# Kernel tuning notes

Hardware: AMD Instinct MI355X
Metric: run time of the kernel (lower is better)

## Reference

```python
import jax, jax.numpy as jnp
import numpy as np

N = 50000
E = 800000
IN_DIM, HID_DIM, EMB_DIM = 128, 256, 128


def _sage_conv(x, src, dst, Wp, bp, Wl, bl, Wr):
    # PyG SAGEConv(project=True, aggr='max'):
    #   x_proj = relu(x @ Wp + bp)            # projection before message passing
    #   aggr   = scatter_max(x_proj[src] -> dst)  (empty segments -> 0)
    #   out    = aggr @ Wl + bl + x @ Wr      # lin_l(aggr) + lin_r(root)
    x_proj = jax.nn.relu(x @ Wp + bp)                      # [N, in]
    msg = x_proj[src]                                      # [E, in] gather
    aggr = jax.ops.segment_max(msg, dst, num_segments=N)   # [N, in] scatter-max
    aggr = jnp.where(jnp.isneginf(aggr), 0.0, aggr)        # empty neighborhoods -> 0
    return aggr @ Wl + bl + x @ Wr


def setup_inputs() -> dict:
    key = jax.random.key(0)
    ks = jax.random.split(key, 12)
    s = 0.05
    return {
        "x": jax.random.normal(ks[0], (N, IN_DIM), dtype=jnp.float32),
        "edge_index": jax.random.randint(ks[1], (2, E), 0, N, dtype=jnp.int64),
        # layer 1 params
        "Wp1": jax.random.normal(ks[2], (IN_DIM, IN_DIM), dtype=jnp.float32) * s,
        "bp1": jnp.zeros((IN_DIM,), dtype=jnp.float32),
        "Wl1": jax.random.normal(ks[3], (IN_DIM, HID_DIM), dtype=jnp.float32) * s,
        "bl1": jnp.zeros((HID_DIM,), dtype=jnp.float32),
        "Wr1": jax.random.normal(ks[4], (IN_DIM, HID_DIM), dtype=jnp.float32) * s,
        # layer 2 params
        "Wp2": jax.random.normal(ks[5], (HID_DIM, HID_DIM), dtype=jnp.float32) * s,
        "bp2": jnp.zeros((HID_DIM,), dtype=jnp.float32),
        "Wl2": jax.random.normal(ks[6], (HID_DIM, EMB_DIM), dtype=jnp.float32) * s,
        "bl2": jnp.zeros((EMB_DIM,), dtype=jnp.float32),
        "Wr2": jax.random.normal(ks[7], (HID_DIM, EMB_DIM), dtype=jnp.float32) * s,
    }


def reference(x, edge_index, Wp1, bp1, Wl1, bl1, Wr1, Wp2, bp2, Wl2, bl2, Wr2):
    src, dst = edge_index[0], edge_index[1]
    h = jax.nn.relu(_sage_conv(x, src, dst, Wp1, bp1, Wl1, bl1, Wr1))
    h = jax.nn.relu(_sage_conv(h, src, dst, Wp2, bp2, Wl2, bl2, Wr2))
    return h
```

## Files before the change

kernel.cpp:

```cpp
#include <hip/hip_runtime.h>


typedef __attribute__((ext_vector_type(8))) short short8;
typedef __attribute__((ext_vector_type(4))) float f32x4;

#define ADJ_CAP 64

__device__ __forceinline__ unsigned short f2bf(float f) {
    unsigned int u = __float_as_uint(f);
    u += 0x7fffu + ((u >> 16) & 1u);
    return (unsigned short)(u >> 16);
}

__device__ __forceinline__ unsigned int pkmax(unsigned int a, unsigned int b) {
    unsigned int r;
    asm("v_pk_max_u16 %0, %1, %2" : "=v"(r) : "v"(a), "v"(b));
    return r;
}

__device__ __forceinline__ short8 pack8(const float4 f0, const float4 f1) {
    union { unsigned short u[8]; short8 v; } r;
    r.u[0] = f2bf(f0.x); r.u[1] = f2bf(f0.y); r.u[2] = f2bf(f0.z); r.u[3] = f2bf(f0.w);
    r.u[4] = f2bf(f1.x); r.u[5] = f2bf(f1.y); r.u[6] = f2bf(f1.z); r.u[7] = f2bf(f1.w);
    return r.v;
}

__global__ __launch_bounds__(256) void pack_all_kernel(
    const float* __restrict__ Wp1, const float* __restrict__ Wl1,
    const float* __restrict__ Wr1, const float* __restrict__ Wp2,
    const float* __restrict__ Wl2, const float* __restrict__ Wr2,
    unsigned short* __restrict__ P0, unsigned short* __restrict__ P1,
    unsigned short* __restrict__ P2, unsigned short* __restrict__ P3,
    unsigned short* __restrict__ P4, unsigned short* __restrict__ P5)
{
    const int idx = blockIdx.x * 256 + threadIdx.x;
    const float* W; unsigned short* P; int Nc, local;
    if      (idx <  16384) { W = Wp1; P = P0; Nc = 128; local = idx; }
    else if (idx <  49152) { W = Wl1; P = P1; Nc = 256; local = idx - 16384; }
    else if (idx <  81920) { W = Wr1; P = P2; Nc = 256; local = idx - 49152; }
    else if (idx < 147456) { W = Wp2; P = P3; Nc = 256; local = idx - 81920; }
    else if (idx < 180224) { W = Wl2; P = P4; Nc = 128; local = idx - 147456; }
    else if (idx < 212992) { W = Wr2; P = P5; Nc = 128; local = idx - 180224; }
    else return;
    const int k = local / Nc, c = local % Nc;
    P[((size_t)(k >> 3) * Nc + c) * 8 + (k & 7)] = f2bf(W[local]);
}

__global__ __launch_bounds__(256) void build_adj_kernel(
    const int* __restrict__ src, const int* __restrict__ dst,
    int* __restrict__ deg, int* __restrict__ padj, int E)
{
    const int e = blockIdx.x * 256 + threadIdx.x;
    if (e < E) {
        const int d = dst[e];
        const int pos = atomicAdd(&deg[d], 1);
        if (pos < ADJ_CAP) padj[(size_t)d * ADJ_CAP + pos] = src[e];
    }
}

template<int K, bool DUAL, bool A_F32, bool B_F32, bool OUT_BF16>
__global__ __launch_bounds__(256) void gemm_ks(
    const void* __restrict__ Ap, const void* __restrict__ Bp,
    const unsigned short* __restrict__ Wl,
    const unsigned short* __restrict__ Wr,
    const float* __restrict__ bias,
    void* __restrict__ outp, int M, int N)
{
    constexpr int LDK = K + 8;
    constexpr int CH  = K / 8;
    __shared__ unsigned short As[64 * LDK];

    const int tid  = threadIdx.x;
    const int lane = tid & 63;
    const int wave = tid >> 6;
    const int fr   = lane & 15;
    const int g    = lane >> 4;
    const int bm   = blockIdx.x * 64;
    const int bn   = blockIdx.y * 128;
    const int wc   = bn + wave * 32;

    const f32x4 zero = {0.f, 0.f, 0.f, 0.f};
    f32x4 acc[4][2];
#pragma unroll
    for (int m = 0; m < 4; ++m)
#pragma unroll
        for (int n = 0; n < 2; ++n) acc[m][n] = zero;

#pragma unroll
    for (int ph = 0; ph < (DUAL ? 2 : 1); ++ph) {
        if (ph) __syncthreads();
        const bool f32src = ph ? B_F32 : A_F32;
        const void* __restrict__ S = ph ? Bp : Ap;
#pragma unroll
        for (int c = 0; c < K / 32; ++c) {
            const int t = tid + c * 256;
            const int r = t / CH, q = t % CH;
            const int gm = min(bm + r, M - 1);
            short8 v;
            if (f32src) {
                const float* Sf = (const float*)S;
                const float4 f0 = *reinterpret_cast<const float4*>(Sf + (size_t)gm * K + q * 8);
                const float4 f1 = *reinterpret_cast<const float4*>(Sf + (size_t)gm * K + q * 8 + 4);
                v = pack8(f0, f1);
            } else {
                v = *reinterpret_cast<const short8*>((const unsigned short*)S + (size_t)gm * K + q * 8);
            }
            *reinterpret_cast<short8*>(&As[r * LDK + q * 8]) = v;
        }
        __syncthreads();
        const unsigned short* __restrict__ W = ph ? Wr : Wl;
#pragma unroll
        for (int kt = 0; kt < K / 32; ++kt) {
            short8 af[4];
#pragma unroll
            for (int m = 0; m < 4; ++m)
                af[m] = *reinterpret_cast<const short8*>(
                    &As[(m * 16 + fr) * LDK + kt * 32 + g * 8]);
#pragma unroll
            for (int n = 0; n < 2; ++n) {
                const short8 bf = *reinterpret_cast<const short8*>(
                    W + ((size_t)(kt * 4 + g) * N + wc + n * 16 + fr) * 8);
#pragma unroll
                for (int m = 0; m < 4; ++m)
                    acc[m][n] = __builtin_amdgcn_mfma_f32_16x16x32_bf16(
                        af[m], bf, acc[m][n], 0, 0, 0);
            }
        }
    }

    float bv[2];
#pragma unroll
    for (int n = 0; n < 2; ++n) bv[n] = bias[wc + n * 16 + fr];
#pragma unroll
    for (int m = 0; m < 4; ++m)
#pragma unroll
        for (int j = 0; j < 4; ++j) {
            const int row = bm + m * 16 + g * 4 + j;
            if (row < M) {
#pragma unroll
                for (int n = 0; n < 2; ++n) {
                    const float v = fmaxf(acc[m][n][j] + bv[n], 0.f);
                    const size_t o = (size_t)row * N + wc + n * 16 + fr;
                    if (OUT_BF16) ((unsigned short*)outp)[o] = f2bf(v);
                    else          ((float*)outp)[o]          = v;
                }
            }
        }
}

template<int D>
__global__ __launch_bounds__(256) void gather_max_bf16(
    const unsigned short* __restrict__ p, const int* __restrict__ padj,
    const int* __restrict__ deg, unsigned short* __restrict__ aggr, int n)
{
    const int node = (blockIdx.x * 256 + threadIdx.x) >> 6;
    const int lane = threadIdx.x & 63;
    if (node >= n) return;
    int d = deg[node];
    if (d > ADJ_CAP) d = ADJ_CAP;
    const int* __restrict__ a = padj + (size_t)node * ADJ_CAP;

    if (D == 128) {
        const int q  = lane >> 4;
        const int ll = lane & 15;
        uint4 acc = make_uint4(0u, 0u, 0u, 0u);
        for (int e = 0; e < d; e += 16) {
            const int i0 = min(e + q,      d - 1);
            const int i1 = min(e + 4 + q,  d - 1);
            const int i2 = min(e + 8 + q,  d - 1);
            const int i3 = min(e + 12 + q, d - 1);
            const int r0 = a[i0], r1 = a[i1], r2 = a[i2], r3 = a[i3];
            const uint4 v0 = *reinterpret_cast<const uint4*>(p + (size_t)r0 * 128 + ll * 8);
            const uint4 v1 = *reinterpret_cast<const uint4*>(p + (size_t)r1 * 128 + ll * 8);
            const uint4 v2 = *reinterpret_cast<const uint4*>(p + (size_t)r2 * 128 + ll * 8);
            const uint4 v3 = *reinterpret_cast<const uint4*>(p + (size_t)r3 * 128 + ll * 8);
            acc.x = pkmax(acc.x, pkmax(pkmax(v0.x, v1.x), pkmax(v2.x, v3.x)));
            acc.y = pkmax(acc.y, pkmax(pkmax(v0.y, v1.y), pkmax(v2.y, v3.y)));
            acc.z = pkmax(acc.z, pkmax(pkmax(v0.z, v1.z), pkmax(v2.z, v3.z)));
            acc.w = pkmax(acc.w, pkmax(pkmax(v0.w, v1.w), pkmax(v2.w, v3.w)));
        }
        acc.x = pkmax(acc.x, (unsigned int)__shfl_xor((int)acc.x, 16, 64));
        acc.y = pkmax(acc.y, (unsigned int)__shfl_xor((int)acc.y, 16, 64));
        acc.z = pkmax(acc.z, (unsigned int)__shfl_xor((int)acc.z, 16, 64));
        acc.w = pkmax(acc.w, (unsigned int)__shfl_xor((int)acc.w, 16, 64));
        acc.x = pkmax(acc.x, (unsigned int)__shfl_xor((int)acc.x, 32, 64));
        acc.y = pkmax(acc.y, (unsigned int)__shfl_xor((int)acc.y, 32, 64));
        acc.z = pkmax(acc.z, (unsigned int)__shfl_xor((int)acc.z, 32, 64));
        acc.w = pkmax(acc.w, (unsigned int)__shfl_xor((int)acc.w, 32, 64));
        if (lane < 16)
            *reinterpret_cast<uint4*>(aggr + (size_t)node * 128 + ll * 8) = acc;
    } else {
        const int h  = lane >> 5;
        const int ll = lane & 31;
        uint4 acc = make_uint4(0u, 0u, 0u, 0u);
        for (int e = 0; e < d; e += 16) {
            const int i0 = min(e + h,      d - 1);
            const int i1 = min(e + 2 + h,  d - 1);
            const int i2 = min(e + 4 + h,  d - 1);
            const int i3 = min(e + 6 + h,  d - 1);
            const int i4 = min(e + 8 + h,  d - 1);
            const int i5 = min(e + 10 + h, d - 1);
            const int i6 = min(e + 12 + h, d - 1);
            const int i7 = min(e + 14 + h, d - 1);
            const int r0 = a[i0], r1 = a[i1], r2 = a[i2], r3 = a[i3];
            const int r4 = a[i4], r5 = a[i5], r6 = a[i6], r7 = a[i7];
            const uint4 v0 = *reinterpret_cast<const uint4*>(p + (size_t)r0 * 256 + ll * 8);
            const uint4 v1 = *reinterpret_cast<const uint4*>(p + (size_t)r1 * 256 + ll * 8);
            const uint4 v2 = *reinterpret_cast<const uint4*>(p + (size_t)r2 * 256 + ll * 8);
            const uint4 v3 = *reinterpret_cast<const uint4*>(p + (size_t)r3 * 256 + ll * 8);
            const uint4 v4 = *reinterpret_cast<const uint4*>(p + (size_t)r4 * 256 + ll * 8);
            const uint4 v5 = *reinterpret_cast<const uint4*>(p + (size_t)r5 * 256 + ll * 8);
            const uint4 v6 = *reinterpret_cast<const uint4*>(p + (size_t)r6 * 256 + ll * 8);
            const uint4 v7 = *reinterpret_cast<const uint4*>(p + (size_t)r7 * 256 + ll * 8);
            acc.x = pkmax(acc.x, pkmax(pkmax(pkmax(v0.x, v1.x), pkmax(v2.x, v3.x)),
                                        pkmax(pkmax(v4.x, v5.x), pkmax(v6.x, v7.x))));
            acc.y = pkmax(acc.y, pkmax(pkmax(pkmax(v0.y, v1.y), pkmax(v2.y, v3.y)),
                                        pkmax(pkmax(v4.y, v5.y), pkmax(v6.y, v7.y))));
            acc.z = pkmax(acc.z, pkmax(pkmax(pkmax(v0.z, v1.z), pkmax(v2.z, v3.z)),
                                        pkmax(pkmax(v4.z, v5.z), pkmax(v6.z, v7.z))));
            acc.w = pkmax(acc.w, pkmax(pkmax(pkmax(v0.w, v1.w), pkmax(v2.w, v3.w)),
                                        pkmax(pkmax(v4.w, v5.w), pkmax(v6.w, v7.w))));
        }
        acc.x = pkmax(acc.x, (unsigned int)__shfl_xor((int)acc.x, 32, 64));
        acc.y = pkmax(acc.y, (unsigned int)__shfl_xor((int)acc.y, 32, 64));
        acc.z = pkmax(acc.z, (unsigned int)__shfl_xor((int)acc.z, 32, 64));
        acc.w = pkmax(acc.w, (unsigned int)__shfl_xor((int)acc.w, 32, 64));
        if (lane < 32)
            *reinterpret_cast<uint4*>(aggr + (size_t)node * 256 + ll * 8) = acc;
    }
}

extern "C" void kernel_launch(void* const* d_in, const int* in_sizes, int n_in,
                              void* d_out, int out_size, void* d_ws, size_t ws_size,
                              hipStream_t stream)
{
    const float* x   = (const float*)d_in[0];
    const int*   ei  = (const int*)d_in[1];
    const float* Wp1 = (const float*)d_in[2];
    const float* bp1 = (const float*)d_in[3];
    const float* Wl1 = (const float*)d_in[4];
    const float* bl1 = (const float*)d_in[5];
    const float* Wr1 = (const float*)d_in[6];
    const float* Wp2 = (const float*)d_in[7];
    const float* bp2 = (const float*)d_in[8];
    const float* Wl2 = (const float*)d_in[9];
    const float* bl2 = (const float*)d_in[10];
    const float* Wr2 = (const float*)d_in[11];
    float* out = (float*)d_out;

    const int M = in_sizes[0] / 128;
    const int E = in_sizes[1] / 2;
    const int* src = ei;
    const int* dst = ei + E;

    unsigned short* ws  = (unsigned short*)d_ws;
    unsigned short* p1b = ws;
    unsigned short* a1b = p1b + (size_t)M * 128;
    unsigned short* h1b = a1b + (size_t)M * 128;
    unsigned short* p2b = h1b + (size_t)M * 256;
    unsigned short* a2b = p2b + (size_t)M * 256;
    unsigned short* wpk = a2b + (size_t)M * 256;
    unsigned short* Wp1p = wpk;
    unsigned short* Wl1p = Wp1p + 128 * 128;
    unsigned short* Wr1p = Wl1p + 128 * 256;
    unsigned short* Wp2p = Wr1p + 128 * 256;
    unsigned short* Wl2p = Wp2p + 256 * 256;
    unsigned short* Wr2p = Wl2p + 256 * 128;
    unsigned short* endu = Wr2p + 256 * 128;
    size_t int_off = ((size_t)(endu - ws) * 2 + 15) & ~(size_t)15;
    int* padj = (int*)((char*)d_ws + int_off);
    int* deg  = padj + (size_t)M * ADJ_CAP;

    const dim3 blk(256);
    const int eb = (E + 255) / 256;
    const int gb = (M + 3) / 4;
    const int mb64 = (M + 63) / 64;

    pack_all_kernel<<<(212992 + 255) / 256, blk, 0, stream>>>(
        Wp1, Wl1, Wr1, Wp2, Wl2, Wr2, Wp1p, Wl1p, Wr1p, Wp2p, Wl2p, Wr2p);
    hipMemsetAsync(deg, 0, (size_t)M * sizeof(int), stream);
    build_adj_kernel<<<eb, blk, 0, stream>>>(src, dst, deg, padj, E);

    gemm_ks<128, false, true, false, true><<<dim3(mb64, 1), blk, 0, stream>>>(
        x, nullptr, Wp1p, nullptr, bp1, p1b, M, 128);
    gather_max_bf16<128><<<gb, blk, 0, stream>>>(p1b, padj, deg, a1b, M);
    gemm_ks<128, true, false, true, true><<<dim3(mb64, 2), blk, 0, stream>>>(
        a1b, x, Wl1p, Wr1p, bl1, h1b, M, 256);

    gemm_ks<256, false, false, false, true><<<dim3(mb64, 2), blk, 0, stream>>>(
        h1b, nullptr, Wp2p, nullptr, bp2, p2b, M, 256);
    gather_max_bf16<256><<<gb, blk, 0, stream>>>(p2b, padj, deg, a2b, M);
    gemm_ks<256, true, false, false, false><<<dim3(mb64, 1), blk, 0, stream>>>(
        a2b, h1b, Wl2p, Wr2p, bl2, out, M, 128);
}
```

Baseline: 212.0 us.

## Overlap root-term GEMMs with neighbor max-gathers in shared kernel launches

Splits each dual GEMM so the x@Wr / h@Wr root term is computed in the same launch as the max-gather, with GEMM blocks and gather blocks sharing one grid. Partial GEMM results are stored as bf16 MFMA fragments and added back in the following lin_l GEMM. The aim is to hide the memory-bound gather behind compute-bound GEMM work and to shrink the shared-memory tile to 128 columns for better occupancy. It adds an extra fragment write/read and rounds the partial sums to bf16, losing some precision.

Result: slower. 220.7 us (+4.1%).

```diff
diff --git a/kernel.cpp b/kernel.cpp
--- a/kernel.cpp
+++ b/kernel.cpp
@@ -58,79 +58,94 @@
     }
 }
 
-template<int K, bool DUAL, bool A_F32, bool B_F32, bool OUT_BF16>
-__global__ __launch_bounds__(256) void gemm_ks(
-    const void* __restrict__ Ap, const void* __restrict__ Bp,
-    const unsigned short* __restrict__ Wl,
-    const unsigned short* __restrict__ Wr,
-    const float* __restrict__ bias,
-    void* __restrict__ outp, int M, int N)
-{
-    constexpr int LDK = K + 8;
-    constexpr int CH  = K / 8;
-    __shared__ unsigned short As[64 * LDK];
-
-    const int tid  = threadIdx.x;
-    const int lane = tid & 63;
-    const int wave = tid >> 6;
-    const int fr   = lane & 15;
-    const int g    = lane >> 4;
-    const int bm   = blockIdx.x * 64;
-    const int bn   = blockIdx.y * 128;
-    const int wc   = bn + wave * 32;
-
-    const f32x4 zero = {0.f, 0.f, 0.f, 0.f};
-    f32x4 acc[4][2];
-#pragma unroll
-    for (int m = 0; m < 4; ++m)
-#pragma unroll
-        for (int n = 0; n < 2; ++n) acc[m][n] = zero;
-
-#pragma unroll
-    for (int ph = 0; ph < (DUAL ? 2 : 1); ++ph) {
-        if (ph) __syncthreads();
-        const bool f32src = ph ? B_F32 : A_F32;
-        const void* __restrict__ S = ph ? Bp : Ap;
-#pragma unroll
-        for (int c = 0; c < K / 32; ++c) {
+template<int K, bool A_F32>
+__device__ __forceinline__ void mfma_accum(
+    const void* __restrict__ S, const unsigned short* __restrict__ W,
+    int M, int N, int bm, int wcol, unsigned short* As,
+    f32x4 (&acc)[4][2], int tid, int fr, int g)
+{
+    constexpr int LDK = 136;
+#pragma unroll
+    for (int half = 0; half < K / 128; ++half) {
+        if (half) __syncthreads();
+#pragma unroll
+        for (int c = 0; c < 4; ++c) {
             const int t = tid + c * 256;
-            const int r = t / CH, q = t % CH;
+            const int r = t >> 4, q = t & 15;
             const int gm = min(bm + r, M - 1);
             short8 v;
-            if (f32src) {
+            if (A_F32) {
                 const float* Sf = (const float*)S;
-                const float4 f0 = *reinterpret_cast<const float4*>(Sf + (size_t)gm * K + q * 8);
-                const float4 f1 = *reinterpret_cast<const float4*>(Sf + (size_t)gm * K + q * 8 + 4);
+                const float4 f0 = *reinterpret_cast<const float4*>(Sf + (size_t)gm * K + half * 128 + q * 8);
+                const float4 f1 = *reinterpret_cast<const float4*>(Sf + (size_t)gm * K + half * 128 + q * 8 + 4);
                 v = pack8(f0, f1);
             } else {
-                v = *reinterpret_cast<const short8*>((const unsigned short*)S + (size_t)gm * K + q * 8);
+                v = *reinterpret_cast<const short8*>((const unsigned short*)S + (size_t)gm * K + half * 128 + q * 8);
             }
             *reinterpret_cast<short8*>(&As[r * LDK + q * 8]) = v;
         }
         __syncthreads();
-        const unsigned short* __restrict__ W = ph ? Wr : Wl;
-#pragma unroll
-        for (int kt = 0; kt < K / 32; ++kt) {
+#pragma unroll
+        for (int kt = 0; kt < 4; ++kt) {
             short8 af[4];
 #pragma unroll
             for (int m = 0; m < 4; ++m)
-                af[m] = *reinterpret_cast<const short8*>(
-                    &As[(m * 16 + fr) * LDK + kt * 32 + g * 8]);
+                af[m] = *reinterpret_cast<const short8*>(&As[(m * 16 + fr) * LDK + kt * 32 + g * 8]);
 #pragma unroll
             for (int n = 0; n < 2; ++n) {
                 const short8 bf = *reinterpret_cast<const short8*>(
-                    W + ((size_t)(kt * 4 + g) * N + wc + n * 16 + fr) * 8);
+                    W + ((size_t)(half * 16 + kt * 4 + g) * N + wcol + n * 16 + fr) * 8);
 #pragma unroll
                 for (int m = 0; m < 4; ++m)
-                    acc[m][n] = __builtin_amdgcn_mfma_f32_16x16x32_bf16(
-                        af[m], bf, acc[m][n], 0, 0, 0);
+                    acc[m][n] = __builtin_amdgcn_mfma_f32_16x16x32_bf16(af[m], bf, acc[m][n], 0, 0, 0);
             }
         }
     }
-
+}
+
+__device__ __forceinline__ void frag_dump(
+    unsigned int* __restrict__ fragOut, int blin, int wave, int lane, f32x4 (&acc)[4][2])
+{
+    unsigned int u[16];
+#pragma unroll
+    for (int t = 0; t < 16; ++t) {
+        const int v0 = 2 * t, n = v0 >> 4, m = (v0 >> 2) & 3, j = v0 & 3;
+        u[t] = (unsigned int)f2bf(acc[m][n][j]) | ((unsigned int)f2bf(acc[m][n][j + 1]) << 16);
+    }
+    unsigned int* seg = fragOut + (((size_t)blin * 4 + wave) << 10);
+#pragma unroll
+    for (int c = 0; c < 4; ++c) {
+        uint4 w; w.x = u[4*c]; w.y = u[4*c+1]; w.z = u[4*c+2]; w.w = u[4*c+3];
+        *reinterpret_cast<uint4*>(seg + c * 256 + lane * 4) = w;
+    }
+}
+
+__device__ __forceinline__ void frag_add(
+    const unsigned int* __restrict__ fragIn, int blin, int wave, int lane, f32x4 (&acc)[4][2])
+{
+    const unsigned int* seg = fragIn + (((size_t)blin * 4 + wave) << 10);
+    unsigned int u[16];
+#pragma unroll
+    for (int c = 0; c < 4; ++c) {
+        const uint4 w = *reinterpret_cast<const uint4*>(seg + c * 256 + lane * 4);
+        u[4*c] = w.x; u[4*c+1] = w.y; u[4*c+2] = w.z; u[4*c+3] = w.w;
+    }
+#pragma unroll
+    for (int v = 0; v < 32; ++v) {
+        const int t = v >> 1, n = v >> 4, m = (v >> 2) & 3, j = v & 3;
+        const unsigned int b = (v & 1) ? (u[t] >> 16) : (u[t] & 0xffffu);
+        acc[m][n][j] += __uint_as_float(b << 16);
+    }
+}
+
+template<bool OUT_BF16>
+__device__ __forceinline__ void bias_relu_store(
+    const float* __restrict__ bias, void* __restrict__ outp,
+    int M, int N, int bm, int wcol, int fr, int g, f32x4 (&acc)[4][2])
+{
     float bv[2];
 #pragma unroll
-    for (int n = 0; n < 2; ++n) bv[n] = bias[wc + n * 16 + fr];
+    for (int n = 0; n < 2; ++n) bv[n] = bias[wcol + n * 16 + fr];
 #pragma unroll
     for (int m = 0; m < 4; ++m)
 #pragma unroll
@@ -140,7 +155,7 @@
 #pragma unroll
                 for (int n = 0; n < 2; ++n) {
                     const float v = fmaxf(acc[m][n][j] + bv[n], 0.f);
-                    const size_t o = (size_t)row * N + wc + n * 16 + fr;
+                    const size_t o = (size_t)row * N + wcol + n * 16 + fr;
                     if (OUT_BF16) ((unsigned short*)outp)[o] = f2bf(v);
                     else          ((float*)outp)[o]          = v;
                 }
@@ -149,12 +164,11 @@
 }
 
 template<int D>
-__global__ __launch_bounds__(256) void gather_max_bf16(
+__device__ __forceinline__ void gather_body(
     const unsigned short* __restrict__ p, const int* __restrict__ padj,
-    const int* __restrict__ deg, unsigned short* __restrict__ aggr, int n)
-{
-    const int node = (blockIdx.x * 256 + threadIdx.x) >> 6;
-    const int lane = threadIdx.x & 63;
+    const int* __restrict__ deg, unsigned short* __restrict__ aggr,
+    int n, int node, int lane)
+{
     if (node >= n) return;
     int d = deg[node];
     if (d > ADJ_CAP) d = ADJ_CAP;
@@ -230,6 +244,124 @@
     }
 }
 
+__global__ __launch_bounds__(256) void p1_kernel(
+    const float* __restrict__ x, const unsigned short* __restrict__ W,
+    const float* __restrict__ bias, unsigned short* __restrict__ p1, int M)
+{
+    __shared__ unsigned short As[64 * 136];
+    const int tid = threadIdx.x, lane = tid & 63, wave = tid >> 6;
+    const int fr = lane & 15, g = lane >> 4;
+    const int bm = blockIdx.x * 64, wcol = wave * 32;
+    f32x4 acc[4][2];
+    const f32x4 zero = {0.f, 0.f, 0.f, 0.f};
+#pragma unroll
+    for (int m = 0; m < 4; ++m) { acc[m][0] = zero; acc[m][1] = zero; }
+    mfma_accum<128, true>(x, W, M, 128, bm, wcol, As, acc, tid, fr, g);
+    bias_relu_store<true>(bias, p1, M, 128, bm, wcol, fr, g, acc);
+}
+
+__global__ __launch_bounds__(256) void g1_kernel(
+    const float* __restrict__ x, const unsigned short* __restrict__ Wr1,
+    unsigned int* __restrict__ xrf,
+    const unsigned short* __restrict__ p1, const int* __restrict__ padj,
+    const int* __restrict__ deg, unsigned short* __restrict__ a1,
+    int M, int nG)
+{
+    __shared__ unsigned short As[64 * 136];
+    const int tid = threadIdx.x, lane = tid & 63, wave = tid >> 6;
+    if ((int)blockIdx.x < nG) {
+        const int bx = blockIdx.x >> 1, by = blockIdx.x & 1;
+        const int fr = lane & 15, g = lane >> 4;
+        f32x4 acc[4][2];
+        const f32x4 zero = {0.f, 0.f, 0.f, 0.f};
+#pragma unroll
+        for (int m = 0; m < 4; ++m) { acc[m][0] = zero; acc[m][1] = zero; }
+        mfma_accum<128, true>(x, Wr1, M, 256, bx * 64, by * 128 + wave * 32, As, acc, tid, fr, g);
+        frag_dump(xrf, bx * 2 + by, wave, lane, acc);
+    } else {
+        const int node = ((int)blockIdx.x - nG) * 4 + wave;
+        gather_body<128>(p1, padj, deg, a1, M, node, lane);
+    }
+}
+
+__global__ __launch_bounds__(256) void h_kernel(
+    const unsigned short* __restrict__ a1, const unsigned short* __restrict__ Wl1,
+    const unsigned int* __restrict__ xrf, const float* __restrict__ bl1,
+    unsigned short* __restrict__ h1, int M)
+{
+    __shared__ unsigned short As[64 * 136];
+    const int tid = threadIdx.x, lane = tid & 63, wave = tid >> 6;
+    const int fr = lane & 15, g = lane >> 4;
+    const int bm = blockIdx.x * 64, by = blockIdx.y;
+    const int wcol = by * 128 + wave * 32;
+    f32x4 acc[4][2];
+    const f32x4 zero = {0.f, 0.f, 0.f, 0.f};
+#pragma unroll
+    for (int m = 0; m < 4; ++m) { acc[m][0] = zero; acc[m][1] = zero; }
+    mfma_accum<128, false>(a1, Wl1, M, 256, bm, wcol, As, acc, tid, fr, g);
+    frag_add(xrf, blockIdx.x * 2 + by, wave, lane, acc);
+    bias_relu_store<true>(bl1, h1, M, 256, bm, wcol, fr, g, acc);
+}
+
+__global__ __launch_bounds__(256) void p2_kernel(
+    const unsigned short* __restrict__ h1, const unsigned short* __restrict__ W,
+    const float* __restrict__ bias, unsigned short* __restrict__ p2, int M)
+{
+    __shared__ unsigned short As[64 * 136];
+    const int tid = threadIdx.x, lane = tid & 63, wave = tid >> 6;
+    const int fr = lane & 15, g = lane >> 4;
+    const int bm = blockIdx.x * 64;
+    const int wcol = blockIdx.y * 128 + wave * 32;
+    f32x4 acc[4][2];
+    const f32x4 zero = {0.f, 0.f, 0.f, 0.f};
+#pragma unroll
+    for (int m = 0; m < 4; ++m) { acc[m][0] = zero; acc[m][1] = zero; }
+    mfma_accum<256, false>(h1, W, M, 256, bm, wcol, As, acc, tid, fr, g);
+    bias_relu_store<true>(bias, p2, M, 256, bm, wcol, fr, g, acc);
+}
+
+__global__ __launch_bounds__(256) void g2_kernel(
+    const unsigned short* __restrict__ h1, const unsigned short* __restrict__ Wr2,
+    unsigned int* __restrict__ orf,
+    const unsigned short* __restrict__ p2, const int* __restrict__ padj,
+    const int* __restrict__ deg, unsigned short* __restrict__ a2,
+    int M, int nG)
+{
+    __shared__ unsigned short As[64 * 136];
+    const int tid = threadIdx.x, lane = tid & 63, wave = tid >> 6;
+    if ((int)blockIdx.x < nG) {
+        const int bx = blockIdx.x;
+        const int fr = lane & 15, g = lane >> 4;
+        f32x4 acc[4][2];
+        const f32x4 zero = {0.f, 0.f, 0.f, 0.f};
+#pragma unroll
+        for (int m = 0; m < 4; ++m) { acc[m][0] = zero; acc[m][1] = zero; }
+        mfma_accum<256, false>(h1, Wr2, M, 128, bx * 64, wave * 32, As, acc, tid, fr, g);
+        frag_dump(orf, bx, wave, lane, acc);
+    } else {
+        const int node = ((int)blockIdx.x - nG) * 4 + wave;
+        gather_body<256>(p2, padj, deg, a2, M, node, lane);
+    }
+}
+
+__global__ __launch_bounds__(256) void out_kernel(
+    const unsigned short* __restrict__ a2, const unsigned short* __restrict__ Wl2,
+    const unsigned int* __restrict__ orf, const float* __restrict__ bl2,
+    float* __restrict__ out, int M)
+{
+    __shared__ unsigned short As[64 * 136];
+    const int tid = threadIdx.x, lane = tid & 63, wave = tid >> 6;
+    const int fr = lane & 15, g = lane >> 4;
+    const int bm = blockIdx.x * 64, wcol = wave * 32;
+    f32x4 acc[4][2];
+    const f32x4 zero = {0.f, 0.f, 0.f, 0.f};
+#pragma unroll
+    for (int m = 0; m < 4; ++m) { acc[m][0] = zero; acc[m][1] = zero; }
+    mfma_accum<256, false>(a2, Wl2, M, 128, bm, wcol, As, acc, tid, fr, g);
+    frag_add(orf, blockIdx.x, wave, lane, acc);
+    bias_relu_store<false>(bl2, out, M, 128, bm, wcol, fr, g, acc);
+}
+
 extern "C" void kernel_launch(void* const* d_in, const int* in_sizes, int n_in,
                               void* d_out, int out_size, void* d_ws, size_t ws_size,
                               hipStream_t stream)
@@ -252,44 +384,50 @@
     const int E = in_sizes[1] / 2;
     const int* src = ei;
     const int* dst = ei + E;
-
-    unsigned short* ws  = (unsigned short*)d_ws;
-    unsigned short* p1b = ws;
-    unsigned short* a1b = p1b + (size_t)M * 128;
-    unsigned short* h1b = a1b + (size_t)M * 128;
-    unsigned short* p2b = h1b + (size_t)M * 256;
-    unsigned short* a2b = p2b + (size_t)M * 256;
-    unsigned short* wpk = a2b + (size_t)M * 256;
-    unsigned short* Wp1p = wpk;
+    const int mb64 = (M + 63) / 64;
+
+    char* B = (char*)d_ws;
+    const size_t szD128 = (size_t)M * 128 * 2;
+    const size_t szD256 = (size_t)M * 256 * 2;
+    const size_t xrBytes = (size_t)mb64 * 2 * 4 * 64 * 16 * 4;
+    const size_t slotA  = (szD256 > xrBytes ? szD256 : xrBytes);
+
+    unsigned short* p1b = (unsigned short*)(B);
+    unsigned short* a1b = (unsigned short*)(B + szD128);
+    unsigned short* h1b = (unsigned short*)(B + 2 * szD128);
+    unsigned short* p2b = (unsigned short*)(B + 2 * szD128 + szD256);
+    unsigned short* a2b = (unsigned short*)(B + 2 * szD128 + 2 * szD256);
+    unsigned int*   xrf = (unsigned int*)  (B + 2 * szD128 + 2 * szD256);
+    unsigned int*   orf = (unsigned int*)  (B);
+    size_t off = 2 * szD128 + 2 * szD256 + slotA;
+    off = (off + 15) & ~(size_t)15;
+    unsigned short* Wp1p = (unsigned short*)(B + off);
     unsigned short* Wl1p = Wp1p + 128 * 128;
     unsigned short* Wr1p = Wl1p + 128 * 256;
     unsigned short* Wp2p = Wr1p + 128 * 256;
     unsigned short* Wl2p = Wp2p + 256 * 256;
     unsigned short* Wr2p = Wl2p + 256 * 128;
-    unsigned short* endu = Wr2p + 256 * 128;
-    size_t int_off = ((size_t)(endu - ws) * 2 + 15) & ~(size_t)15;
-    int* padj = (int*)((char*)d_ws + int_off);
+    size_t off2 = off + 2 * (size_t)(16384 + 32768 * 2 + 65536 + 32768 * 2);
+    off2 = (off2 + 15) & ~(size_t)15;
+    int* padj = (int*)(B + off2);
     int* deg  = padj + (size_t)M * ADJ_CAP;
 
     const dim3 blk(256);
     const int eb = (E + 255) / 256;
     const int gb = (M + 3) / 4;
-    const int mb64 = (M + 63) / 64;
 
     pack_all_kernel<<<(212992 + 255) / 256, blk, 0, stream>>>(
         Wp1, Wl1, Wr1, Wp2, Wl2, Wr2, Wp1p, Wl1p, Wr1p, Wp2p, Wl2p, Wr2p);
     hipMemsetAsync(deg, 0, (size_t)M * sizeof(int), stream);
     build_adj_kernel<<<eb, blk, 0, stream>>>(src, dst, deg, padj, E);
 
-    gemm_ks<128, false, true, false, true><<<dim3(mb64, 1), blk, 0, stream>>>(
-        x, nullptr, Wp1p, nullptr, bp1, p1b, M, 128);
-    gather_max_bf16<128><<<gb, blk, 0, stream>>>(p1b, padj, deg, a1b, M);
-    gemm_ks<128, true, false, true, true><<<dim3(mb64, 2), blk, 0, stream>>>(
-        a1b, x, Wl1p, Wr1p, bl1, h1b, M, 256);
-
-    gemm_ks<256, false, false, false, true><<<dim3(mb64, 2), blk, 0, stream>>>(
-        h1b, nullptr, Wp2p, nullptr, bp2, p2b, M, 256);
-    gather_max_bf16<256><<<gb, blk, 0, stream>>>(p2b, padj, deg, a2b, M);
-    gemm_ks<256, true, false, false, false><<<dim3(mb64, 1), blk, 0, stream>>>(
-        a2b, h1b, Wl2p, Wr2p, bl2, out, M, 128);
-}
+    p1_kernel<<<mb64, blk, 0, stream>>>(x, Wp1p, bp1, p1b, M);
+    g1_kernel<<<mb64 * 2 + gb, blk, 0, stream>>>(
+        x, Wr1p, xrf, p1b, padj, deg, a1b, M, mb64 * 2);
+    h_kernel<<<dim3(mb64, 2), blk, 0, stream>>>(a1b, Wl1p, xrf, bl1, h1b, M);
+
+    p2_kernel<<<dim3(mb64, 2), blk, 0, stream>>>(h1b, Wp2p, bp2, p2b, M);
+    g2_kernel<<<mb64 + gb, blk, 0, stream>>>(
+        h1b, Wr2p, orf, p2b, padj, deg, a2b, M, mb64);
+    out_kernel<<<mb64, blk, 0, stream>>>(a2b, Wl2p, orf, bl2, out, M);
+}
```
